# Performance work log

Measured on AMD Instinct MI355X. Metric: run time of the kernel, lower is better.

The kernel has to match this reference:

```python
import jax, jax.numpy as jnp
import numpy as np

N = 50000
E = 800000
C_IN = 64
C_OUT = 64
K = 3  # Chebyshev order (num_stacks)
LAMBDA_MAX = 2.0


def setup_inputs() -> dict:
    key = jax.random.key(0)
    ks = jax.random.split(key, 32)
    inp = {
        'X': jax.random.normal(ks[0], (N, C_IN), dtype=jnp.float32),
        'edge_index': jax.random.randint(ks[1], (2, E), 0, N, dtype=jnp.int64),
        'edge_weight': jax.random.uniform(ks[2], (E,), dtype=jnp.float32),
        'H': jax.random.normal(ks[3], (N, C_OUT), dtype=jnp.float32),
        'C': jax.random.normal(ks[4], (N, C_OUT), dtype=jnp.float32),
    }
    # 8 ChebConvs: conv_{x,h}_{i,f,c,o}; x-convs map C_IN->C_OUT, h-convs C_OUT->C_OUT
    names_x = ['Wxi', 'Wxf', 'Wxc', 'Wxo']
    names_h = ['Whi', 'Whf', 'Whc', 'Who']
    i = 5
    for nx, nh in zip(names_x, names_h):
        inp[nx] = jax.random.normal(ks[i], (K, C_IN, C_OUT), dtype=jnp.float32) * (1.0 / np.sqrt(K * C_IN)); i += 1
        inp['b' + nx[1:]] = jax.random.normal(ks[i], (C_OUT,), dtype=jnp.float32) * 0.01; i += 1
        inp[nh] = jax.random.normal(ks[i], (K, C_OUT, C_OUT), dtype=jnp.float32) * (1.0 / np.sqrt(K * C_OUT)); i += 1
        inp['b' + nh[1:]] = jax.random.normal(ks[i], (C_OUT,), dtype=jnp.float32) * 0.01; i += 1
    # per-gate biases b_i, b_f, b_c, b_o of shape [1, C_OUT] (zero-initialized in torch)
    for nm in ['bi', 'bf', 'bc', 'bo']:
        inp[nm] = jax.random.normal(ks[i], (1, C_OUT), dtype=jnp.float32) * 0.01; i += 1
    return inp


def _cheb_norm(edge_index, edge_weight, n):
    # symmetric normalization: D^-1/2 W D^-1/2 (PyG get_laplacian 'sym')
    row, col = edge_index[0], edge_index[1]
    deg = jax.ops.segment_sum(edge_weight, row, num_segments=n)
    dinv = jnp.where(deg > 0, jax.lax.rsqrt(jnp.where(deg > 0, deg, 1.0)), 0.0)
    return dinv[row] * edge_weight * dinv[col]


def _cheb_conv(x, W, b, row, col, nw, n):
    # ChebConv: out = sum_k T_k(L_hat) x @ W[k] + b, with
    # L_hat v = (2/lambda_max) * (v - A_norm v) - v
    def Lhat(v):
        agg = jax.ops.segment_sum(nw[:, None] * v[col], row, num_segments=n)
        return (2.0 / LAMBDA_MAX) * (v - agg) - v
    Tx_prev = x
    out = x @ W[0]
    k = W.shape[0]
    if k > 1:
        Tx = Lhat(x)
        out = out + Tx @ W[1]
        for j in range(2, k):
            Tx_new = 2.0 * Lhat(Tx) - Tx_prev
            out = out + Tx_new @ W[j]
            Tx_prev, Tx = Tx, Tx_new
    return out + b


def reference(X, edge_index, edge_weight, H, C,
              Wxi, bxi, Whi, bhi, Wxf, bxf, Whf, bhf,
              Wxc, bxc, Whc, bhc, Wxo, bxo, Who, bho,
              bi, bf, bc, bo):
    n = X.shape[0]
    row, col = edge_index[0], edge_index[1]
    nw = _cheb_norm(edge_index, edge_weight, n)
    cc = lambda v, W, b: _cheb_conv(v, W, b, row, col, nw, n)
    I = jax.nn.sigmoid(cc(X, Wxi, bxi) + cc(H, Whi, bhi) + bi)
    F = jax.nn.sigmoid(cc(X, Wxf, bxf) + cc(H, Whf, bhf) + bf)
    T = jnp.tanh(cc(X, Wxc, bxc) + cc(H, Whc, bhc) + bc)
    C_new = F * C + I * T
    O = jax.nn.sigmoid(cc(X, Wxo, bxo) + cc(H, Who, bho) + bo)
    H_new = O * jnp.tanh(C_new)
    return (H_new, C_new)
```

## Files before the change

kernel.cpp:

```cpp
#include <hip/hip_runtime.h>

#define N_NODES 50000
#define N_PAD   50048
#define N_EDGES 800000
#define NBE4    782
#define NB_IL2  1563
#define NBKT    196
#define BCAP    4992
#define NCHUNK  4

typedef __attribute__((ext_vector_type(8))) short bf16x8;
typedef __attribute__((ext_vector_type(4))) float f32x4;

__device__ __forceinline__ unsigned short f2bf(float f) {
    unsigned u = __float_as_uint(f);
    u = (u + 0x7fffu + ((u >> 16) & 1u)) >> 16;
    return (unsigned short)u;
}

__device__ __forceinline__ float fsig(float x) {
    x = fminf(fmaxf(x, -30.f), 30.f);
    float t = __expf(x);
    return __fdividef(t, 1.f + t);
}
__device__ __forceinline__ float ftanh(float x) {
    x = fminf(fmaxf(x, -15.f), 15.f);
    float t = __expf(2.f * x);
    return 1.f - __fdividef(2.f, t + 1.f);
}


__global__ __launch_bounds__(256) void k_prep(
    const void* __restrict__ eiraw,
    unsigned* __restrict__ hist,
    const float* __restrict__ X, const float* __restrict__ H, unsigned short* __restrict__ XH,
    const float* __restrict__ Wxi, const float* __restrict__ Whi,
    const float* __restrict__ Wxf, const float* __restrict__ Whf,
    const float* __restrict__ Wxc, const float* __restrict__ Whc,
    const float* __restrict__ Wxo, const float* __restrict__ Who,
    const float* __restrict__ bxi, const float* __restrict__ bhi,
    const float* __restrict__ bxf, const float* __restrict__ bhf,
    const float* __restrict__ bxc, const float* __restrict__ bhc,
    const float* __restrict__ bxo, const float* __restrict__ bho,
    const float* __restrict__ bgi, const float* __restrict__ bgf,
    const float* __restrict__ bgc, const float* __restrict__ bgo,
    unsigned short* __restrict__ Wf, float* __restrict__ ball) {
    __shared__ int sflag;
    __shared__ unsigned cnt[NBKT];
    int b = blockIdx.x, t = threadIdx.x;
    if (b < NBE4) {
        if (t == 0) sflag = 0;
        if (t < NBKT) cnt[t] = 0;
        __syncthreads();
        int si = b * 1024 + t;
        int sv = ((const int*)eiraw)[1 + 2 * si];
        if (sv) atomicOr(&sflag, 1);
        __syncthreads();
        int is32 = sflag;
#pragma unroll
        for (int k = 0; k < 4; k++) {
            int e = b * 1024 + k * 256 + t;
            if (e < N_EDGES) {
                int r = is32 ? ((const int*)eiraw)[e] : (int)(((const long long*)eiraw)[e]);
                atomicAdd(&cnt[r >> 8], 1u);
            }
        }
        __syncthreads();
        if (t < NBKT) hist[(size_t)t * NBE4 + b] = cnt[t];
        return;
    }
    int bb = b - NBE4;
    if (bb < NB_IL2) {
        int tt = bb * 256 + t;
        int node = tt >> 3, g = tt & 7;
        if (node >= N_NODES) return;
        const float* base = (g < 4) ? (X + (size_t)node * 64 + g * 16)
                                    : (H + (size_t)node * 64 + (g - 4) * 16);
        float4 v0 = ((const float4*)base)[0];
        float4 v1 = ((const float4*)base)[1];
        float4 v2 = ((const float4*)base)[2];
        float4 v3 = ((const float4*)base)[3];
        uint4 o0, o1;
        o0.x = (unsigned)f2bf(v0.x) | ((unsigned)f2bf(v0.y) << 16);
        o0.y = (unsigned)f2bf(v0.z) | ((unsigned)f2bf(v0.w) << 16);
        o0.z = (unsigned)f2bf(v1.x) | ((unsigned)f2bf(v1.y) << 16);
        o0.w = (unsigned)f2bf(v1.z) | ((unsigned)f2bf(v1.w) << 16);
        o1.x = (unsigned)f2bf(v2.x) | ((unsigned)f2bf(v2.y) << 16);
        o1.y = (unsigned)f2bf(v2.z) | ((unsigned)f2bf(v2.w) << 16);
        o1.z = (unsigned)f2bf(v3.x) | ((unsigned)f2bf(v3.y) << 16);
        o1.w = (unsigned)f2bf(v3.z) | ((unsigned)f2bf(v3.w) << 16);
        unsigned short* dst = XH + (size_t)node * 128 + g * 16;
        *(uint4*)dst = o0;
        *(uint4*)(dst + 8) = o1;
        return;
    }
    bb -= NB_IL2;
    if (bb < 48) {
        int flat = bb * 256 + t;
        int l = flat & 63, nt = (flat >> 6) & 15, ks = flat >> 10;
        int n = nt * 16 + (l & 15);
        int g = n >> 6, c = n & 63;
        const float* WX = (g == 0) ? Wxi : (g == 1) ? Wxf : (g == 2) ? Wxc : Wxo;
        const float* WH = (g == 0) ? Whi : (g == 1) ? Whf : (g == 2) ? Whc : Who;
        int k0 = ks * 32 + (l >> 4) * 8;
        unsigned short ov[8];
#pragma unroll
        for (int j = 0; j < 8; j++) {
            int k = k0 + j;
            int bsel = k >> 7, ch = k & 127;
            const float* W = (ch < 64) ? WX : WH;
            int kk = ch & 63;
            float v;
            if (bsel == 0)      v = W[kk * 64 + c] - W[2 * 4096 + kk * 64 + c];
            else if (bsel == 1) v = -W[4096 + kk * 64 + c];
            else                v = 2.f * W[2 * 4096 + kk * 64 + c];
            ov[j] = f2bf(v);
        }
        uint4 o;
        o.x = (unsigned)ov[0] | ((unsigned)ov[1] << 16);
        o.y = (unsigned)ov[2] | ((unsigned)ov[3] << 16);
        o.z = (unsigned)ov[4] | ((unsigned)ov[5] << 16);
        o.w = (unsigned)ov[6] | ((unsigned)ov[7] << 16);
        *(uint4*)(Wf + (size_t)flat * 8) = o;
    } else {
        int g = t >> 6, c = t & 63;
        const float* BX = (g == 0) ? bxi : (g == 1) ? bxf : (g == 2) ? bxc : bxo;
        const float* BH = (g == 0) ? bhi : (g == 1) ? bhf : (g == 2) ? bhc : bho;
        const float* BG = (g == 0) ? bgi : (g == 1) ? bgf : (g == 2) ? bgc : bgo;
        ball[t] = BX[c] + BH[c] + BG[c];
    }
}


__global__ __launch_bounds__(256) void k_bscan(unsigned* __restrict__ hist, unsigned* __restrict__ btot) {
    __shared__ unsigned s[256];
    int j = blockIdx.x, t = threadIdx.x;
    unsigned* row = hist + (size_t)j * NBE4;
    unsigned v[4];
#pragma unroll
    for (int k = 0; k < 4; k++) {
        int i = t * 4 + k;
        v[k] = (i < NBE4) ? row[i] : 0u;
    }
    unsigned tsum = v[0] + v[1] + v[2] + v[3];
    s[t] = tsum; __syncthreads();
    for (int d = 1; d < 256; d <<= 1) {
        unsigned a = (t >= d) ? s[t - d] : 0u;
        __syncthreads();
        s[t] += a;
        __syncthreads();
    }
    unsigned run = s[t] - tsum;
#pragma unroll
    for (int k = 0; k < 4; k++) {
        int i = t * 4 + k;
        if (i < NBE4) { unsigned c = v[k]; row[i] = run; run += c; }
    }
    if (t == 255) btot[j] = s[255];
}


__global__ __launch_bounds__(256) void k_scat(const void* __restrict__ eiraw, const float* __restrict__ w,
                                              const unsigned* __restrict__ hist, const unsigned* __restrict__ btot,
                                              unsigned long long* __restrict__ ebuf) {
    __shared__ int sflag;
    __shared__ unsigned ssc[256];
    __shared__ unsigned boff[NBKT];
    __shared__ unsigned cur[NBKT];
    int b = blockIdx.x, t = threadIdx.x;
    unsigned v = (t < NBKT) ? btot[t] : 0u;
    ssc[t] = v; __syncthreads();
    for (int d = 1; d < 256; d <<= 1) {
        unsigned a = (t >= d) ? ssc[t - d] : 0u;
        __syncthreads();
        ssc[t] += a;
        __syncthreads();
    }
    if (t < NBKT) { boff[t] = (ssc[t] - v) + hist[(size_t)t * NBE4 + b]; cur[t] = 0u; }
    if (t == 0) sflag = 0;
    __syncthreads();
    int si = b * 1024 + t;
    int sv = ((const int*)eiraw)[1 + 2 * si];
    if (sv) atomicOr(&sflag, 1);
    __syncthreads();
    int is32 = sflag;
#pragma unroll
    for (int k = 0; k < 4; k++) {
        int e = b * 1024 + k * 256 + t;
        if (e < N_EDGES) {
            int r, c;
            if (is32) { r = ((const int*)eiraw)[e]; c = ((const int*)eiraw)[N_EDGES + e]; }
            else      { r = (int)(((const long long*)eiraw)[e]); c = (int)(((const long long*)eiraw)[N_EDGES + e]); }
            float wv = w[e];
            int bk = r >> 8;
            unsigned lr = atomicAdd(&cur[bk], 1u);
            unsigned pos = boff[bk] + lr;
            ebuf[pos] = ((unsigned long long)(unsigned)r << 48)
                      | (((unsigned long long)(unsigned)c & 0xffffull) << 32)
                      | (unsigned long long)__float_as_uint(wv);
        }
    }
}


__global__ __launch_bounds__(1024) void k_build(const unsigned long long* __restrict__ ebuf,
                                                const unsigned* __restrict__ btot,
                                                int* __restrict__ rp, float* __restrict__ dinv,
                                                int* __restrict__ colp, float* __restrict__ wraw) {
    __shared__ unsigned long long se[BCAP];
    __shared__ unsigned ssc[256];
    __shared__ unsigned cnt[256];
    __shared__ float wsum[256];
    __shared__ unsigned off[256];
    __shared__ unsigned cur[256];
    int b = blockIdx.x, t = threadIdx.x;
    if (t < 256) ssc[t] = (t < NBKT) ? btot[t] : 0u;
    __syncthreads();
    for (int d = 1; d < 256; d <<= 1) {
        unsigned a = 0u;
        if (t < 256 && t >= d) a = ssc[t - d];
        __syncthreads();
        if (t < 256) ssc[t] += a;
        __syncthreads();
    }
    unsigned base = (b > 0) ? ssc[b - 1] : 0u;
    unsigned end  = ssc[b];
    int n = (int)(end - base);
    if (b == 0 && t == 0) rp[N_NODES] = N_EDGES;
    if (t < 256) { cnt[t] = 0u; wsum[t] = 0.f; }
    __syncthreads();
    for (int i = t; i < n; i += 1024) {
        unsigned long long e = ebuf[base + i];
        if (i < BCAP) se[i] = e;
        unsigned lr = (unsigned)(e >> 48) & 255u;
        atomicAdd(&cnt[lr], 1u);
        atomicAdd(&wsum[lr], __uint_as_float((unsigned)(e & 0xffffffffu)));
    }
    __syncthreads();
    if (t < 256) off[t] = cnt[t];
    __syncthreads();
    for (int d = 1; d < 256; d <<= 1) {
        unsigned a = 0u;
        if (t < 256 && t >= d) a = off[t - d];
        __syncthreads();
        if (t < 256) off[t] += a;
        __syncthreads();
    }
    if (t < 256) {
        unsigned excl = off[t] - cnt[t];
        off[t] = excl;
        cur[t] = excl;
        int row = b * 256 + t;
        if (row < N_NODES) {
            rp[row] = (int)(base + excl);
            float dg = wsum[t];
            dinv[row] = (dg > 0.f) ? rsqrtf(dg) : 0.f;
        }
    }
    __syncthreads();
    for (int i = t; i < n; i += 1024) {
        unsigned long long e = (i < BCAP) ? se[i] : ebuf[base + i];
        unsigned lr = (unsigned)(e >> 48) & 255u;
        unsigned p = atomicAdd(&cur[lr], 1u);
        int row = b * 256 + (int)lr;
        int c = (int)((e >> 32) & 0xffffu);
        colp[base + p] = (row << 16) | c;
        wraw[base + p] = __uint_as_float((unsigned)(e & 0xffffffffu));
    }
}


__global__ __launch_bounds__(256) void k_nw(const int* __restrict__ colp, const float* __restrict__ wraw,
                                            const float* __restrict__ dinv, float* __restrict__ nwp) {
    int e = blockIdx.x * 256 + threadIdx.x;
    if (e >= N_EDGES) return;
    unsigned rc = (unsigned)colp[e];
    nwp[e] = dinv[rc >> 16] * wraw[e] * dinv[rc & 0xffffu];
}


__global__ __launch_bounds__(256) void k_spmv_ch(const unsigned short* __restrict__ src,
                                                 unsigned short* __restrict__ dst,
                                                 const int* __restrict__ rp,
                                                 const int* __restrict__ colp, const float* __restrict__ nwp,
                                                 int ch) {
    int t = threadIdx.x;
    int node = blockIdx.x * 16 + (t >> 4);
    int ls = t & 15;
    int cofs = ch * 32;
    int s = rp[node], e = rp[node + 1];
    float a0 = 0.f, a1 = 0.f;
    for (int jb = s; jb < e; jb += 8) {
        int   c[8]; float wv[8]; unsigned vv[8];
#pragma unroll
        for (int k = 0; k < 8; k++) {
            int j = jb + k;
            int jc = (j < e) ? j : (e - 1);
            c[k]  = colp[jc] & 0xffff;
            wv[k] = (j < e) ? nwp[jc] : 0.f;
        }
#pragma unroll
        for (int k = 0; k < 8; k++)
            vv[k] = *(const unsigned*)(src + (size_t)c[k] * 128 + cofs + ls * 2);
#pragma unroll
        for (int k = 0; k < 8; k++) {
            a0 = fmaf(wv[k], __uint_as_float(vv[k] << 16), a0);
            a1 = fmaf(wv[k], __uint_as_float(vv[k] & 0xffff0000u), a1);
        }
    }
    unsigned o = (unsigned)f2bf(a0) | ((unsigned)f2bf(a1) << 16);
    *(unsigned*)(dst + (size_t)node * 128 + cofs + ls * 2) = o;
}


__global__ __launch_bounds__(256) void k_gemm_mfma(
    const unsigned short* __restrict__ XH, const unsigned short* __restrict__ U1,
    const unsigned short* __restrict__ U2, const unsigned short* __restrict__ Wf,
    const float* __restrict__ ball, const float* __restrict__ C, float* __restrict__ out) {
    __shared__ __align__(16) uint4 Bs[2][1024];

    int t = threadIdx.x;
    int wid = t >> 6, lane = t & 63;
    int col = lane & 15, quad = lane >> 4;
    int m0 = blockIdx.x * 64 + wid * 16;
    int arow = m0 + col;

    f32x4 acc[16];
#pragma unroll
    for (int i = 0; i < 16; i++) acc[i] = (f32x4){0.f, 0.f, 0.f, 0.f};

    const unsigned short* srcs[3] = {XH, U1, U2};

    bf16x8 a_cur = *(const bf16x8*)(srcs[0] + (size_t)arow * 128 + quad * 8);
    const uint4* g0 = (const uint4*)Wf;
    uint4 p0 = g0[t], p1 = g0[t + 256], p2 = g0[t + 512], p3 = g0[t + 768];

    for (int ks = 0; ks < 12; ks++) {
        uint4* dstb = Bs[ks & 1];
        dstb[t] = p0; dstb[t + 256] = p1; dstb[t + 512] = p2; dstb[t + 768] = p3;
        __syncthreads();
        bf16x8 a_nxt = a_cur;
        if (ks < 11) {
            int ks1 = ks + 1;
            const uint4* g = (const uint4*)(Wf + (size_t)ks1 * 8192);
            p0 = g[t]; p1 = g[t + 256]; p2 = g[t + 512]; p3 = g[t + 768];
            a_nxt = *(const bf16x8*)(srcs[ks1 >> 2] + (size_t)arow * 128 + (ks1 & 3) * 32 + quad * 8);
        }
        const unsigned short* B = (const unsigned short*)Bs[ks & 1];
#pragma unroll
        for (int nt = 0; nt < 16; nt++) {
            bf16x8 bfrag = *(const bf16x8*)(B + nt * 512 + lane * 8);
            acc[nt] = __builtin_amdgcn_mfma_f32_16x16x32_bf16(a_cur, bfrag, acc[nt], 0, 0, 0);
        }
        a_cur = a_nxt;
    }

    float bI[4], bF[4], bT[4], bO[4];
#pragma unroll
    for (int cq = 0; cq < 4; cq++) {
        int c = cq * 16 + col;
        bI[cq] = ball[c]; bF[cq] = ball[64 + c]; bT[cq] = ball[128 + c]; bO[cq] = ball[192 + c];
    }
#pragma unroll
    for (int r = 0; r < 4; r++) {
        int node = m0 + quad * 4 + r;
        if (node >= N_NODES) continue;
#pragma unroll
        for (int cq = 0; cq < 4; cq++) {
            int c = cq * 16 + col;
            float ig = fsig(acc[0 + cq][r]  + bI[cq]);
            float fg = fsig(acc[4 + cq][r]  + bF[cq]);
            float tg = ftanh(acc[8 + cq][r] + bT[cq]);
            float og = fsig(acc[12 + cq][r] + bO[cq]);
            float cv = fmaf(fg, C[(size_t)node * 64 + c], ig * tg);
            out[(size_t)node * 64 + c] = og * ftanh(cv);
            out[(size_t)N_NODES * 64 + (size_t)node * 64 + c] = cv;
        }
    }
}


extern "C" void kernel_launch(void* const* d_in, const int* in_sizes, int n_in,
                              void* d_out, int out_size, void* d_ws, size_t ws_size,
                              hipStream_t stream) {
    const float* X   = (const float*)d_in[0];
    const void*  ei  = d_in[1];
    const float* w   = (const float*)d_in[2];
    const float* H   = (const float*)d_in[3];
    const float* C   = (const float*)d_in[4];
    const float* Wxi = (const float*)d_in[5];  const float* bxi = (const float*)d_in[6];
    const float* Whi = (const float*)d_in[7];  const float* bhi = (const float*)d_in[8];
    const float* Wxf = (const float*)d_in[9];  const float* bxf = (const float*)d_in[10];
    const float* Whf = (const float*)d_in[11]; const float* bhf = (const float*)d_in[12];
    const float* Wxc = (const float*)d_in[13]; const float* bxc = (const float*)d_in[14];
    const float* Whc = (const float*)d_in[15]; const float* bhc = (const float*)d_in[16];
    const float* Wxo = (const float*)d_in[17]; const float* bxo = (const float*)d_in[18];
    const float* Who = (const float*)d_in[19]; const float* bho = (const float*)d_in[20];
    const float* bgi = (const float*)d_in[21]; const float* bgf = (const float*)d_in[22];
    const float* bgc = (const float*)d_in[23]; const float* bgo = (const float*)d_in[24];
    float* out = (float*)d_out;

    char* ws = (char*)d_ws;
    size_t off = 0;
    auto alloc = [&](size_t bytes) -> char* {
        char* p = ws + off;
        off = (off + bytes + 255) & ~(size_t)255;
        return p;
    };
    unsigned* hist  = (unsigned*)alloc((size_t)NBKT * NBE4 * 4);
    unsigned* btot  = (unsigned*)alloc((NBKT + 1) * 4);
    unsigned long long* ebuf = (unsigned long long*)alloc((size_t)N_EDGES * 8);
    int*   rp   = (int*)alloc((N_NODES + 1) * 4);
    float* dinv = (float*)alloc(N_NODES * 4);
    int*   colp = (int*)alloc((size_t)(N_EDGES + 8) * 4);
    float* wraw = (float*)alloc((size_t)(N_EDGES + 8) * 4);
    float* nwp  = (float*)alloc((size_t)(N_EDGES + 8) * 4);
    unsigned short* XH = (unsigned short*)alloc((size_t)N_PAD * 128 * 2);
    unsigned short* U1 = (unsigned short*)alloc((size_t)N_PAD * 128 * 2);
    unsigned short* U2 = (unsigned short*)alloc((size_t)N_PAD * 128 * 2);
    unsigned short* Wf = (unsigned short*)alloc((size_t)12 * 16 * 64 * 8 * 2);
    float* ball = (float*)alloc(256 * 4);
    (void)ws_size; (void)in_sizes; (void)n_in; (void)out_size;

    k_prep<<<NBE4 + NB_IL2 + 49, 256, 0, stream>>>(ei, hist, X, H, XH,
                                                   Wxi, Whi, Wxf, Whf, Wxc, Whc, Wxo, Who,
                                                   bxi, bhi, bxf, bhf, bxc, bhc, bxo, bho,
                                                   bgi, bgf, bgc, bgo, Wf, ball);
    k_bscan<<<NBKT, 256, 0, stream>>>(hist, btot);
    k_scat<<<NBE4, 256, 0, stream>>>(ei, w, hist, btot, ebuf);
    k_build<<<NBKT, 1024, 0, stream>>>(ebuf, btot, rp, dinv, colp, wraw);
    k_nw<<<(N_EDGES + 255) / 256, 256, 0, stream>>>(colp, wraw, dinv, nwp);
    for (int ch = 0; ch < NCHUNK; ch++) {
        k_spmv_ch<<<N_NODES / 16, 256, 0, stream>>>(XH, U1, rp, colp, nwp, ch);
        k_spmv_ch<<<N_NODES / 16, 256, 0, stream>>>(U1, U2, rp, colp, nwp, ch);
    }
    k_gemm_mfma<<<(N_NODES + 63) / 64, 256, 0, stream>>>(XH, U1, U2, Wf, ball, C, out);
}
```

Before: 320.0 us.

## Replace chunked SpMV with full-row wavefront-per-node SpMV and packed col/weight array

The old SpMV made four 32-column passes per Chebyshev step, with 16 lanes per node. The new kernel gives each node a full 64-lane wavefront covering all 128 bf16 columns in one pass, so there are two launches instead of eight. The normalised weight and column index are packed into one int2 array, so one load fetches both. Each edge index list is now read once per step instead of four times. The trade-off is that the chunking, presumably there to keep the gathered source slice resident in cache, is lost, and gathers now span the whole feature buffer.

```diff
diff --git a/kernel.cpp b/kernel.cpp
--- a/kernel.cpp
+++ b/kernel.cpp
@@ -7,7 +7,6 @@
 #define NB_IL2  1563
 #define NBKT    196
 #define BCAP    4992
-#define NCHUNK  4
 
 typedef __attribute__((ext_vector_type(8))) short bf16x8;
 typedef __attribute__((ext_vector_type(4))) float f32x4;
@@ -271,45 +270,46 @@
 
 
 __global__ __launch_bounds__(256) void k_nw(const int* __restrict__ colp, const float* __restrict__ wraw,
-                                            const float* __restrict__ dinv, float* __restrict__ nwp) {
+                                            const float* __restrict__ dinv, int2* __restrict__ cw) {
     int e = blockIdx.x * 256 + threadIdx.x;
     if (e >= N_EDGES) return;
     unsigned rc = (unsigned)colp[e];
-    nwp[e] = dinv[rc >> 16] * wraw[e] * dinv[rc & 0xffffu];
-}
-
-
-__global__ __launch_bounds__(256) void k_spmv_ch(const unsigned short* __restrict__ src,
+    int c = (int)(rc & 0xffffu);
+    float nw = dinv[rc >> 16] * wraw[e] * dinv[c];
+    cw[e] = make_int2(c, __float_as_int(nw));
+}
+
+
+__global__ __launch_bounds__(256) void k_spmv_bf(const unsigned short* __restrict__ src,
                                                  unsigned short* __restrict__ dst,
                                                  const int* __restrict__ rp,
-                                                 const int* __restrict__ colp, const float* __restrict__ nwp,
-                                                 int ch) {
-    int t = threadIdx.x;
-    int node = blockIdx.x * 16 + (t >> 4);
-    int ls = t & 15;
-    int cofs = ch * 32;
+                                                 const int2* __restrict__ cw) {
+    int wid = threadIdx.x >> 6, lane = threadIdx.x & 63;
+    int node = blockIdx.x * 4 + wid;
+    if (node >= N_NODES) return;
     int s = rp[node], e = rp[node + 1];
     float a0 = 0.f, a1 = 0.f;
-    for (int jb = s; jb < e; jb += 8) {
-        int   c[8]; float wv[8]; unsigned vv[8];
-#pragma unroll
-        for (int k = 0; k < 8; k++) {
+    for (int jb = s; jb < e; jb += 16) {
+        int2 cv[16]; unsigned vv[16];
+#pragma unroll
+        for (int k = 0; k < 16; k++) {
             int j = jb + k;
             int jc = (j < e) ? j : (e - 1);
-            c[k]  = colp[jc] & 0xffff;
-            wv[k] = (j < e) ? nwp[jc] : 0.f;
-        }
-#pragma unroll
-        for (int k = 0; k < 8; k++)
-            vv[k] = *(const unsigned*)(src + (size_t)c[k] * 128 + cofs + ls * 2);
-#pragma unroll
-        for (int k = 0; k < 8; k++) {
-            a0 = fmaf(wv[k], __uint_as_float(vv[k] << 16), a0);
-            a1 = fmaf(wv[k], __uint_as_float(vv[k] & 0xffff0000u), a1);
+            cv[k] = cw[jc];
+            if (j >= e) cv[k].y = 0;
+        }
+#pragma unroll
+        for (int k = 0; k < 16; k++)
+            vv[k] = *(const unsigned*)(src + (size_t)cv[k].x * 128 + lane * 2);
+#pragma unroll
+        for (int k = 0; k < 16; k++) {
+            float wv = __int_as_float(cv[k].y);
+            a0 = fmaf(wv, __uint_as_float(vv[k] << 16), a0);
+            a1 = fmaf(wv, __uint_as_float(vv[k] & 0xffff0000u), a1);
         }
     }
     unsigned o = (unsigned)f2bf(a0) | ((unsigned)f2bf(a1) << 16);
-    *(unsigned*)(dst + (size_t)node * 128 + cofs + ls * 2) = o;
+    *(unsigned*)(dst + (size_t)node * 128 + lane * 2) = o;
 }
 
 
@@ -414,7 +414,7 @@
     float* dinv = (float*)alloc(N_NODES * 4);
     int*   colp = (int*)alloc((size_t)(N_EDGES + 8) * 4);
     float* wraw = (float*)alloc((size_t)(N_EDGES + 8) * 4);
-    float* nwp  = (float*)alloc((size_t)(N_EDGES + 8) * 4);
+    int2*  cw   = (int2*)alloc((size_t)(N_EDGES + 16) * 8);
     unsigned short* XH = (unsigned short*)alloc((size_t)N_PAD * 128 * 2);
     unsigned short* U1 = (unsigned short*)alloc((size_t)N_PAD * 128 * 2);
     unsigned short* U2 = (unsigned short*)alloc((size_t)N_PAD * 128 * 2);
@@ -429,10 +429,8 @@
     k_bscan<<<NBKT, 256, 0, stream>>>(hist, btot);
     k_scat<<<NBE4, 256, 0, stream>>>(ei, w, hist, btot, ebuf);
     k_build<<<NBKT, 1024, 0, stream>>>(ebuf, btot, rp, dinv, colp, wraw);
-    k_nw<<<(N_EDGES + 255) / 256, 256, 0, stream>>>(colp, wraw, dinv, nwp);
-    for (int ch = 0; ch < NCHUNK; ch++) {
-        k_spmv_ch<<<N_NODES / 16, 256, 0, stream>>>(XH, U1, rp, colp, nwp, ch);
-        k_spmv_ch<<<N_NODES / 16, 256, 0, stream>>>(U1, U2, rp, colp, nwp, ch);
-    }
+    k_nw<<<(N_EDGES + 255) / 256, 256, 0, stream>>>(colp, wraw, dinv, cw);
+    k_spmv_bf<<<(N_NODES + 3) / 4, 256, 0, stream>>>(XH, U1, rp, cw);
+    k_spmv_bf<<<(N_NODES + 3) / 4, 256, 0, stream>>>(U1, U2, rp, cw);
     k_gemm_mfma<<<(N_NODES + 63) / 64, 256, 0, stream>>>(XH, U1, U2, Wf, ball, C, out);
 }
```

Result: faster. 302.5 us (-5.5%).
